# Kernel optimization log

Hardware: AMD Instinct MI355X
Metric: run time of the kernel (lower is better)

Reference implementation:

```python
import jax, jax.numpy as jnp
import numpy as np

B, S, D, H = 4, 2048, 1024, 16
DK = D // H


def setup_inputs() -> dict:
    key = jax.random.key(0)
    ks = jax.random.split(key, 11)
    std = 1.0 / np.sqrt(D)
    mk = lambda k: jax.random.uniform(k, (D, D), jnp.float32, -std, std)
    mb = lambda k: jax.random.uniform(k, (D,), jnp.float32, -std, std)
    return {
        "query": jax.random.normal(ks[0], (B, S, D), jnp.float32),
        "key": jax.random.normal(ks[1], (B, S, D), jnp.float32),
        "value": jax.random.normal(ks[2], (B, S, D), jnp.float32),
        "Wq": mk(ks[3]), "bq": mb(ks[4]),
        "Wk": mk(ks[5]), "bk": mb(ks[6]),
        "Wv": mk(ks[7]), "bv": mb(ks[8]),
        "Wo": mk(ks[9]), "bo": mb(ks[10]),
    }


def reference(query, key, value, Wq, bq, Wk, bk, Wv, bv, Wo, bo):
    # Linear projections (torch Linear: x @ W.T + b)
    Q = query @ Wq.T + bq   # [B,S,D]
    K = key @ Wk.T + bk
    V = value @ Wv.T + bv
    # split heads -> [B,H,S,DK]
    Q = Q.reshape(B, S, H, DK).transpose(0, 2, 1, 3)
    K = K.reshape(B, S, H, DK).transpose(0, 2, 1, 3)
    V = V.reshape(B, S, H, DK).transpose(0, 2, 1, 3)
    scale = 1.0 / jnp.sqrt(jnp.asarray(DK, Q.dtype))
    scores = jnp.einsum("bhqd,bhkd->bhqk", Q, K) * scale  # [B,H,S,S]
    attn = jax.nn.softmax(scores, axis=-1)
    out = jnp.einsum("bhqk,bhkd->bhqd", attn, V)          # [B,H,S,DK]
    out = out.transpose(0, 2, 1, 3).reshape(B, S, D)       # [B,S,D]
    return out @ Wo.T + bo
```

## Files before the change

### kernel.cpp

```cpp
#include <hip/hip_runtime.h>
#include <hip/hip_bf16.h>
#include <stdint.h>


using f32x4  = __attribute__((ext_vector_type(4))) float;
using f32x16 = __attribute__((ext_vector_type(16))) float;
using s16x8  = __attribute__((ext_vector_type(8))) short;
using u16x8  = __attribute__((ext_vector_type(8))) unsigned short;
using u16x4  = __attribute__((ext_vector_type(4))) unsigned short;

#define MFMA16(a, b, c) __builtin_amdgcn_mfma_f32_16x16x32_bf16((a), (b), (c), 0, 0, 0)
#define MFMA32(a, b, c) __builtin_amdgcn_mfma_f32_32x32x16_bf16((a), (b), (c), 0, 0, 0)

#define GLL16(gptr, lptr)                                                      \
  __builtin_amdgcn_global_load_lds(                                            \
      (const __attribute__((address_space(1))) void*)(gptr),                   \
      (__attribute__((address_space(3))) void*)(lptr), 16, 0, 0)

__device__ __forceinline__ unsigned short f2bf(float f) {
  union { __hip_bfloat16 h; unsigned short u; } cv;
  cv.h = __float2bfloat16(f);
  return cv.u;
}

__device__ __forceinline__ unsigned int pkrne(float a, float b) {
  unsigned int ua = __builtin_bit_cast(unsigned int, a);
  unsigned int ub = __builtin_bit_cast(unsigned int, b);
  ua = ua + 0x7FFFu + ((ua >> 16) & 1u);
  ub = ub + 0x7FFFu + ((ub >> 16) & 1u);
  return __builtin_amdgcn_perm(ub, ua, 0x07060302u);
}

__device__ __forceinline__ float exp2a(float x) {
  return __builtin_amdgcn_exp2f(x);
}

__global__ __launch_bounds__(256) void cast_all_kernel(
    const float* __restrict__ wq, const float* __restrict__ wk,
    const float* __restrict__ wv, const float* __restrict__ wo,
    const float* __restrict__ xq, const float* __restrict__ xk,
    const float* __restrict__ xv, unsigned short* __restrict__ wbf,
    unsigned short* __restrict__ oxq, unsigned short* __restrict__ oxk,
    unsigned short* __restrict__ oxv) {
  const int job = blockIdx.y;
  const int i = blockIdx.x * 256 + threadIdx.x;
  const float* src;
  unsigned short* dst;
  size_t off;
  if (job < 4) {
    src = (job == 0) ? wq : (job == 1) ? wk : (job == 2) ? wv : wo;
    dst = wbf + (size_t)job * 1048576;
    off = (size_t)i;
  } else {
    const int xi = job - 4, z = xi >> 3, sl = xi & 7;
    src = (z == 0) ? xq : (z == 1) ? xk : xv;
    dst = (z == 0) ? oxq : (z == 1) ? oxk : oxv;
    off = (size_t)sl * 262144 + i;
  }
  float4 f = reinterpret_cast<const float4*>(src)[off];
  uint2 p;
  p.x = pkrne(f.x, f.y);
  p.y = pkrne(f.z, f.w);
  *reinterpret_cast<uint2*>(dst + off * 4) = p;
}

__global__ __launch_bounds__(256) void gemm_qkvv_kernel(
    const unsigned short* __restrict__ Xq, const unsigned short* __restrict__ Xk,
    const unsigned short* __restrict__ Xv, const unsigned short* __restrict__ wbf,
    const float* __restrict__ bq, const float* __restrict__ bk,
    const float* __restrict__ bv, unsigned short* __restrict__ Qh,
    unsigned short* __restrict__ Kh, unsigned short* __restrict__ Vh) {
  const int z = blockIdx.z;
  const unsigned short* Xbf = (z == 0) ? Xq : (z == 1) ? Xk : Xv;
  const unsigned short* W = wbf + (size_t)z * 1048576;
  const float* bias = (z == 0) ? bq : (z == 1) ? bk : bv;
  const float qscale = (z == 0) ? 0.18033688011112042f : 1.0f;

  __shared__ __align__(16) unsigned short Asm_[128 * 64];
  __shared__ __align__(16) unsigned short Bsm_[128 * 64];

  const int t = threadIdx.x;
  const int lane = t & 63, w = t >> 6;
  const int g = lane >> 4, c = lane & 15;
  const int wm = (w >> 1) * 64, wn = (w & 1) * 64;
  const int n0 = (blockIdx.y & 7) * 128;
  const int m0 = (blockIdx.x * 8 + (blockIdx.y >> 3)) * 128;

  f32x4 acc[4][4];
#pragma unroll
  for (int i = 0; i < 4; i++)
#pragma unroll
    for (int j = 0; j < 4; j++) acc[i][j] = (f32x4)0.0f;

  const int blr = lane >> 3;
  const int bgc = (lane & 7) ^ blr;

  for (int kt = 0; kt < 16; ++kt) {
    const int k0 = kt * 64;
    __syncthreads();
#pragma unroll
    for (int i = 0; i < 4; i++) {
      int ii = w * 4 + i;
      const unsigned short* ga = Xbf + (size_t)(m0 + ii * 8 + blr) * 1024 + k0 + bgc * 8;
      GLL16(ga, &Asm_[ii * 512]);
      const unsigned short* gb = W + (size_t)(n0 + ii * 8 + blr) * 1024 + k0 + bgc * 8;
      GLL16(gb, &Bsm_[ii * 512]);
    }
    __syncthreads();

#pragma unroll
    for (int ks = 0; ks < 2; ks++) {
      s16x8 af[4], bfr[4];
#pragma unroll
      for (int mt = 0; mt < 4; mt++) {
        int r = wm + mt * 16 + c;
        af[mt] = *reinterpret_cast<const s16x8*>(&Asm_[r * 64 + (((ks * 4 + g) ^ (c & 7)) << 3)]);
      }
#pragma unroll
      for (int nt = 0; nt < 4; nt++) {
        int r = wn + nt * 16 + c;
        bfr[nt] = *reinterpret_cast<const s16x8*>(&Bsm_[r * 64 + (((ks * 4 + g) ^ (c & 7)) << 3)]);
      }
      if (z == 2) {
#pragma unroll
        for (int nt = 0; nt < 4; nt++)
#pragma unroll
          for (int mt = 0; mt < 4; mt++)
            acc[nt][mt] = MFMA16(bfr[nt], af[mt], acc[nt][mt]);
      } else {
#pragma unroll
        for (int mt = 0; mt < 4; mt++)
#pragma unroll
          for (int nt = 0; nt < 4; nt++)
            acc[mt][nt] = MFMA16(af[mt], bfr[nt], acc[mt][nt]);
      }
    }
  }

  if (z == 2) {
#pragma unroll
    for (int nt = 0; nt < 4; nt++)
#pragma unroll
      for (int mt = 0; mt < 4; mt++) {
        int m = m0 + wm + mt * 16 + c;
        int b = m >> 11, s = m & 2047;
#pragma unroll
        for (int r = 0; r < 4; r++) {
          int n = n0 + wn + nt * 16 + g * 4 + r;
          int h = n >> 6, dk = n & 63;
          Vh[(((size_t)b * 16 + h) * 64 + dk) * 2048 + s] =
              f2bf(acc[nt][mt][r] + bv[n]);
        }
      }
  } else {
    unsigned short* dst = (z == 0) ? Qh : Kh;
#pragma unroll
    for (int mt = 0; mt < 4; mt++)
#pragma unroll
      for (int nt = 0; nt < 4; nt++) {
        int n = n0 + wn + nt * 16 + c;
        float bb = bias[n];
        int h = n >> 6, dk = n & 63;
#pragma unroll
        for (int r = 0; r < 4; r++) {
          int m = m0 + wm + mt * 16 + g * 4 + r;
          int b = m >> 11, s = m & 2047;
          dst[(((size_t)b * 16 + h) * 2048 + s) * 64 + dk] =
              f2bf((acc[mt][nt][r] + bb) * qscale);
        }
      }
  }
}

__global__ __launch_bounds__(256) void gemm_out_kernel(
    const unsigned short* __restrict__ AO, const unsigned short* __restrict__ Wo,
    const float* __restrict__ bo, float* __restrict__ out) {
  __shared__ __align__(16) unsigned short Asm_[128 * 64];
  __shared__ __align__(16) unsigned short Bsm_[64 * 64];

  const int t = threadIdx.x;
  const int lane = t & 63, w = t >> 6;
  const int g = lane >> 4, c = lane & 15;
  const int wm = (w >> 1) * 64, wn = (w & 1) * 32;
  const int n0 = (blockIdx.y & 15) * 64;
  const int m0 = (blockIdx.x * 8 + (blockIdx.y >> 4)) * 128;

  f32x4 acc[4][2];
#pragma unroll
  for (int i = 0; i < 4; i++)
#pragma unroll
    for (int j = 0; j < 2; j++) acc[i][j] = (f32x4)0.0f;

  const int blr = lane >> 3;
  const int bgc = (lane & 7) ^ blr;

  for (int kt = 0; kt < 16; ++kt) {
    const int k0 = kt * 64;
    __syncthreads();
#pragma unroll
    for (int i = 0; i < 4; i++) {
      int ii = w * 4 + i;
      const unsigned short* ga = AO + (size_t)(m0 + ii * 8 + blr) * 1024 + k0 + bgc * 8;
      GLL16(ga, &Asm_[ii * 512]);
    }
#pragma unroll
    for (int i = 0; i < 2; i++) {
      int ii = w * 2 + i;
      const unsigned short* gb = Wo + (size_t)(n0 + ii * 8 + blr) * 1024 + k0 + bgc * 8;
      GLL16(gb, &Bsm_[ii * 512]);
    }
    __syncthreads();

#pragma unroll
    for (int ks = 0; ks < 2; ks++) {
      s16x8 af[4], bfr[2];
#pragma unroll
      for (int mt = 0; mt < 4; mt++) {
        int r = wm + mt * 16 + c;
        af[mt] = *reinterpret_cast<const s16x8*>(&Asm_[r * 64 + (((ks * 4 + g) ^ (c & 7)) << 3)]);
      }
#pragma unroll
      for (int nt = 0; nt < 2; nt++) {
        int r = wn + nt * 16 + c;
        bfr[nt] = *reinterpret_cast<const s16x8*>(&Bsm_[r * 64 + (((ks * 4 + g) ^ (c & 7)) << 3)]);
      }
#pragma unroll
      for (int mt = 0; mt < 4; mt++)
#pragma unroll
        for (int nt = 0; nt < 2; nt++)
          acc[mt][nt] = MFMA16(af[mt], bfr[nt], acc[mt][nt]);
    }
  }

#pragma unroll
  for (int mt = 0; mt < 4; mt++)
#pragma unroll
    for (int nt = 0; nt < 2; nt++) {
      int n = n0 + wn + nt * 16 + c;
      float bb = bo[n];
#pragma unroll
      for (int r = 0; r < 4; r++) {
        int m = m0 + wm + mt * 16 + g * 4 + r;
        out[(size_t)m * 1024 + n] = acc[mt][nt][r] + bb;
      }
    }
}

__global__ __launch_bounds__(512) void attn_kernel(
    const unsigned short* __restrict__ Qh, const unsigned short* __restrict__ Kh,
    const unsigned short* __restrict__ Vh, unsigned short* __restrict__ AO) {
  const int bh = blockIdx.x * 8 + (blockIdx.y >> 3);
  const int b = bh >> 4, h = bh & 15;
  const int q0 = (blockIdx.y & 7) * 256;
  const int t = threadIdx.x, lane = t & 63, w = t >> 6;
  const int lo = lane & 31, hi = lane >> 5;

  __shared__ __align__(16) unsigned short Ks[3][64 * 64];
  __shared__ __align__(16) unsigned short Vs[3][64 * 64];

  const size_t kvbase = (size_t)bh * 2048 * 64;

  s16x8 qb[4];
  {
    const unsigned short* qp = Qh + kvbase + (size_t)(q0 + w * 32 + lo) * 64;
#pragma unroll
    for (int ks = 0; ks < 4; ks++)
      qb[ks] = *reinterpret_cast<const s16x8*>(qp + ks * 16 + hi * 8);
  }

  s16x8 onesb;
  {
    uint4 u;
    u.x = 0x3F803F80u; u.y = 0x3F803F80u; u.z = 0x3F803F80u; u.w = 0x3F803F80u;
    onesb = *reinterpret_cast<const s16x8*>(&u);
  }

  f32x16 oacc[2], lacc;
  oacc[0] = (f32x16)0.0f; oacc[1] = (f32x16)0.0f; lacc = (f32x16)0.0f;

  const int srow = t >> 3;
  const int gch = (t & 7) ^ (srow & 7) ^ w;
  const unsigned short* Kg = Kh + kvbase + (size_t)srow * 64 + gch * 8;
  const unsigned short* Vg = Vh + kvbase + (size_t)srow * 2048 + gch * 8;

  const int rx0 = (lo & 7) ^ (lo >> 3);
  const int rx1 = (lo & 7) ^ (4 | (lo >> 3));

  auto stage = [&](int buf, int tile) {
    GLL16(Kg + (size_t)tile * 4096, &Ks[buf][w * 512]);
    GLL16(Vg + tile * 64, &Vs[buf][w * 512]);
  };
  auto qk_tile = [&](int buf, f32x16* st) {
    st[0] = (f32x16)0.0f; st[1] = (f32x16)0.0f;
#pragma unroll
    for (int kb = 0; kb < 2; kb++) {
      const int rx = kb ? rx1 : rx0;
#pragma unroll
      for (int ks = 0; ks < 4; ks++) {
        s16x8 ka = *reinterpret_cast<const s16x8*>(
            &Ks[buf][(kb * 32 + lo) * 64 + (((ks * 2 + hi) ^ rx) << 3)]);
        st[kb] = MFMA32(ka, qb[ks], st[kb]);
      }
    }
  };
  auto sm_pack = [&](const f32x16* st, s16x8* pa) {
#pragma unroll
    for (int kb = 0; kb < 2; kb++) {
      float e[16];
#pragma unroll
      for (int r = 0; r < 16; r++) e[r] = exp2a(st[kb][r]);
#pragma unroll
      for (int half = 0; half < 2; half++) {
        const float* eb = e + half * 8;
        unsigned int x1 = pkrne(eb[0], eb[1]);
        unsigned int x2 = pkrne(eb[2], eb[3]);
        unsigned int y1 = pkrne(eb[4], eb[5]);
        unsigned int y2 = pkrne(eb[6], eb[7]);
        asm volatile("v_permlane32_swap_b32 %0, %1" : "+v"(x1), "+v"(y1));
        asm volatile("v_permlane32_swap_b32 %0, %1" : "+v"(x2), "+v"(y2));
        uint4 u;
        u.x = x1; u.y = x2; u.z = y1; u.w = y2;
        pa[kb * 2 + half] = *reinterpret_cast<const s16x8*>(&u);
      }
    }
  };
  auto pv_tile = [&](int buf, const s16x8* pa) {
#pragma unroll
    for (int ks = 0; ks < 4; ks++) lacc = MFMA32(pa[ks], onesb, lacc);
#pragma unroll
    for (int ks = 0; ks < 4; ks++)
#pragma unroll
      for (int db = 0; db < 2; db++) {
        const int rx = db ? rx1 : rx0;
        s16x8 vb = *reinterpret_cast<const s16x8*>(
            &Vs[buf][(db * 32 + lo) * 64 + (((ks * 2 + hi) ^ rx) << 3)]);
        oacc[db] = MFMA32(pa[ks], vb, oacc[db]);
      }
  };

  s16x8 paA[4], paB[4];

  stage(0, 0);
  __syncthreads();
  stage(1, 1);
  {
    f32x16 st0[2];
    qk_tile(0, st0);
    sm_pack(st0, paA);
  }
  __syncthreads();

  for (int u = 0; u < 16; ++u) {
    const int te = 2 * u;
    if (te + 2 < 32) stage((te + 2) % 3, te + 2);
    {
      f32x16 stn[2];
      qk_tile((te + 1) % 3, stn);
      pv_tile(te % 3, paA);
      sm_pack(stn, paB);
    }
    __syncthreads();

    const int to = te + 1;
    if (to + 2 < 32) stage((to + 2) % 3, to + 2);
    if (to + 1 < 32) {
      f32x16 stn[2];
      qk_tile((to + 1) % 3, stn);
      pv_tile(to % 3, paB);
      sm_pack(stn, paA);
    } else {
      pv_tile(to % 3, paB);
    }
    __syncthreads();
  }

#pragma unroll
  for (int r = 0; r < 16; r++) {
    float inv_r = 1.0f / lacc[r];
    int qr = (r & 3) + ((r >> 2) << 3) + (hi << 2);
    int srow_q = q0 + w * 32 + qr;
    size_t obase = ((size_t)b * 2048 + srow_q) * 1024 + (size_t)h * 64;
    AO[obase + lo]      = f2bf(oacc[0][r] * inv_r);
    AO[obase + 32 + lo] = f2bf(oacc[1][r] * inv_r);
  }
}

extern "C" void kernel_launch(void* const* d_in, const int* in_sizes, int n_in,
                              void* d_out, int out_size, void* d_ws, size_t ws_size,
                              hipStream_t stream) {
  const float* query = (const float*)d_in[0];
  const float* key   = (const float*)d_in[1];
  const float* value = (const float*)d_in[2];
  const float* Wq = (const float*)d_in[3];
  const float* bq = (const float*)d_in[4];
  const float* Wk = (const float*)d_in[5];
  const float* bk = (const float*)d_in[6];
  const float* Wv = (const float*)d_in[7];
  const float* bv = (const float*)d_in[8];
  const float* Wo = (const float*)d_in[9];
  const float* bo = (const float*)d_in[10];

  uint8_t* wsb = (uint8_t*)d_ws;
  unsigned short* wbf = (unsigned short*)wsb;
  unsigned short* Qh  = (unsigned short*)(wsb + 8388608);
  unsigned short* Kh  = (unsigned short*)(wsb + 8388608 + 16777216);
  unsigned short* Vh  = (unsigned short*)(wsb + 8388608 + 2 * 16777216);
  unsigned short* AO  = (unsigned short*)(wsb + 8388608 + 3 * 16777216);
  unsigned short* Xq = AO;
  unsigned short* Xk = (unsigned short*)d_out;
  unsigned short* Xv = (unsigned short*)d_out + 8388608;

  cast_all_kernel<<<dim3(1024, 28), dim3(256), 0, stream>>>(
      Wq, Wk, Wv, Wo, query, key, value, wbf, Xq, Xk, Xv);
  gemm_qkvv_kernel<<<dim3(8, 64, 3), dim3(256), 0, stream>>>(
      Xq, Xk, Xv, wbf, bq, bk, bv, Qh, Kh, Vh);
  attn_kernel<<<dim3(8, 64), dim3(512), 0, stream>>>(Qh, Kh, Vh, AO);
  gemm_out_kernel<<<dim3(8, 128), dim3(256), 0, stream>>>(
      AO, wbf + (size_t)3 * 1048576, bo, (float*)d_out);
}
```

Measured before the change: 230.0 us.

## Shrink attention blocks to 4 waves and use simple double-buffered KV loop

```diff
diff --git a/kernel.cpp b/kernel.cpp
--- a/kernel.cpp
+++ b/kernel.cpp
@@ -246,17 +246,17 @@
     }
 }
 
-__global__ __launch_bounds__(512) void attn_kernel(
+__global__ __launch_bounds__(256) void attn_kernel(
     const unsigned short* __restrict__ Qh, const unsigned short* __restrict__ Kh,
     const unsigned short* __restrict__ Vh, unsigned short* __restrict__ AO) {
-  const int bh = blockIdx.x * 8 + (blockIdx.y >> 3);
+  const int bh = blockIdx.x * 8 + (blockIdx.y >> 4);
   const int b = bh >> 4, h = bh & 15;
-  const int q0 = (blockIdx.y & 7) * 256;
+  const int q0 = (blockIdx.y & 15) * 128;
   const int t = threadIdx.x, lane = t & 63, w = t >> 6;
   const int lo = lane & 31, hi = lane >> 5;
 
-  __shared__ __align__(16) unsigned short Ks[3][64 * 64];
-  __shared__ __align__(16) unsigned short Vs[3][64 * 64];
+  __shared__ __align__(16) unsigned short Ks[2][64 * 64];
+  __shared__ __align__(16) unsigned short Vs[2][64 * 64];
 
   const size_t kvbase = (size_t)bh * 2048 * 64;
 
@@ -278,19 +278,35 @@
   f32x16 oacc[2], lacc;
   oacc[0] = (f32x16)0.0f; oacc[1] = (f32x16)0.0f; lacc = (f32x16)0.0f;
 
-  const int srow = t >> 3;
-  const int gch = (t & 7) ^ (srow & 7) ^ w;
-  const unsigned short* Kg = Kh + kvbase + (size_t)srow * 64 + gch * 8;
-  const unsigned short* Vg = Vh + kvbase + (size_t)srow * 2048 + gch * 8;
+  const int srw = t >> 3;
+  const int gch0 = (t & 7) ^ (srw & 7) ^ w;
+  const unsigned short* Kg0 = Kh + kvbase + (size_t)srw * 64 + gch0 * 8;
+  const unsigned short* Kg1 = Kh + kvbase + (size_t)(32 + srw) * 64 + (gch0 ^ 4) * 8;
+  const unsigned short* Vg0 = Vh + kvbase + (size_t)srw * 2048 + gch0 * 8;
+  const unsigned short* Vg1 = Vh + kvbase + (size_t)(32 + srw) * 2048 + (gch0 ^ 4) * 8;
 
   const int rx0 = (lo & 7) ^ (lo >> 3);
   const int rx1 = (lo & 7) ^ (4 | (lo >> 3));
 
-  auto stage = [&](int buf, int tile) {
-    GLL16(Kg + (size_t)tile * 4096, &Ks[buf][w * 512]);
-    GLL16(Vg + tile * 64, &Vs[buf][w * 512]);
-  };
-  auto qk_tile = [&](int buf, f32x16* st) {
+  GLL16(Kg0, &Ks[0][w * 512]);
+  GLL16(Kg1, &Ks[0][2048 + w * 512]);
+  GLL16(Vg0, &Vs[0][w * 512]);
+  GLL16(Vg1, &Vs[0][2048 + w * 512]);
+  __syncthreads();
+
+  for (int it = 0; it < 32; ++it) {
+    const int cur = it & 1;
+    if (it < 31) {
+      const int nb = cur ^ 1;
+      const size_t ko = (size_t)(it + 1) * 4096;
+      const int vo = (it + 1) * 64;
+      GLL16(Kg0 + ko, &Ks[nb][w * 512]);
+      GLL16(Kg1 + ko, &Ks[nb][2048 + w * 512]);
+      GLL16(Vg0 + vo, &Vs[nb][w * 512]);
+      GLL16(Vg1 + vo, &Vs[nb][2048 + w * 512]);
+    }
+
+    f32x16 st[2];
     st[0] = (f32x16)0.0f; st[1] = (f32x16)0.0f;
 #pragma unroll
     for (int kb = 0; kb < 2; kb++) {
@@ -298,12 +314,12 @@
 #pragma unroll
       for (int ks = 0; ks < 4; ks++) {
         s16x8 ka = *reinterpret_cast<const s16x8*>(
-            &Ks[buf][(kb * 32 + lo) * 64 + (((ks * 2 + hi) ^ rx) << 3)]);
+            &Ks[cur][(kb * 32 + lo) * 64 + (((ks * 2 + hi) ^ rx) << 3)]);
         st[kb] = MFMA32(ka, qb[ks], st[kb]);
       }
     }
-  };
-  auto sm_pack = [&](const f32x16* st, s16x8* pa) {
+
+    s16x8 pa[4];
 #pragma unroll
     for (int kb = 0; kb < 2; kb++) {
       float e[16];
@@ -323,54 +339,20 @@
         pa[kb * 2 + half] = *reinterpret_cast<const s16x8*>(&u);
       }
     }
-  };
-  auto pv_tile = [&](int buf, const s16x8* pa) {
+
 #pragma unroll
     for (int ks = 0; ks < 4; ks++) lacc = MFMA32(pa[ks], onesb, lacc);
+
 #pragma unroll
     for (int ks = 0; ks < 4; ks++)
 #pragma unroll
       for (int db = 0; db < 2; db++) {
         const int rx = db ? rx1 : rx0;
         s16x8 vb = *reinterpret_cast<const s16x8*>(
-            &Vs[buf][(db * 32 + lo) * 64 + (((ks * 2 + hi) ^ rx) << 3)]);
+            &Vs[cur][(db * 32 + lo) * 64 + (((ks * 2 + hi) ^ rx) << 3)]);
         oacc[db] = MFMA32(pa[ks], vb, oacc[db]);
       }
-  };
-
-  s16x8 paA[4], paB[4];
-
-  stage(0, 0);
-  __syncthreads();
-  stage(1, 1);
-  {
-    f32x16 st0[2];
-    qk_tile(0, st0);
-    sm_pack(st0, paA);
-  }
-  __syncthreads();
-
-  for (int u = 0; u < 16; ++u) {
-    const int te = 2 * u;
-    if (te + 2 < 32) stage((te + 2) % 3, te + 2);
-    {
-      f32x16 stn[2];
-      qk_tile((te + 1) % 3, stn);
-      pv_tile(te % 3, paA);
-      sm_pack(stn, paB);
-    }
-    __syncthreads();
-
-    const int to = te + 1;
-    if (to + 2 < 32) stage((to + 2) % 3, to + 2);
-    if (to + 1 < 32) {
-      f32x16 stn[2];
-      qk_tile((to + 1) % 3, stn);
-      pv_tile(to % 3, paB);
-      sm_pack(stn, paA);
-    } else {
-      pv_tile(to % 3, paB);
-    }
+
     __syncthreads();
   }
 
@@ -414,7 +396,7 @@
       Wq, Wk, Wv, Wo, query, key, value, wbf, Xq, Xk, Xv);
   gemm_qkvv_kernel<<<dim3(8, 64, 3), dim3(256), 0, stream>>>(
       Xq, Xk, Xv, wbf, bq, bk, bv, Qh, Kh, Vh);
-  attn_kernel<<<dim3(8, 64), dim3(512), 0, stream>>>(Qh, Kh, Vh, AO);
+  attn_kernel<<<dim3(8, 128), dim3(256), 0, stream>>>(Qh, Kh, Vh, AO);
   gemm_out_kernel<<<dim3(8, 128), dim3(256), 0, stream>>>(
       AO, wbf + (size_t)3 * 1048576, bo, (float*)d_out);
 }
```

Result: faster. 220.4 us (-4.2%).
